# Kernel optimization log

Hardware: AMD Instinct MI355X
Metric: run time of the kernel (lower is better)

The kernel has to match this reference:

```python
import jax, jax.numpy as jnp
import numpy as np
from jax import lax

# Ring of the 8 non-center positions of a 3x3 kernel, cyclic clockwise
# starting at top-middle. A rotation offset 'off' (in 1/8 turns) shifts
# kernel taps around this ring; 'off' = step*rot where step = 8/kernel_rot.
_RING = [(0, 1), (0, 2), (1, 2), (2, 2), (2, 1), (2, 0), (1, 0), (0, 0)]
_CENTER = (1, 1)


def _tap_positions(kernel_type, off):
    """Return list of (row, col) 3x3 positions, one per stored kernel value."""
    if kernel_type == 0:  # skel: 5 taps = 4-point cross (rotated) + center
        pos = [_RING[(2 * k + off) % 8] for k in range(4)] + [_CENTER]
    elif kernel_type == 1:  # full 3x3: 8 ring taps (rotated) + center
        pos = [_RING[(k + off) % 8] for k in range(8)] + [_CENTER]
    else:  # bar: tap - center - opposite tap, rotated
        pos = [_RING[off % 8], _CENTER, _RING[(4 + off) % 8]]
    return pos


def _build_dense_kernel(weight, kernel_type, off):
    # weight: [O, I, num_kernel] -> dense [O, I, 3, 3]
    O, I, nk = weight.shape
    dense = jnp.zeros((O, I, 3, 3), dtype=weight.dtype)
    for k, (r, c) in enumerate(_tap_positions(kernel_type, off)):
        dense = dense.at[:, :, r, c].set(weight[:, :, k])
    return dense


def setup_inputs() -> dict:
    key = jax.random.key(0)
    k1, k2 = jax.random.split(key)
    x_tensor = jax.random.normal(k1, (16, 64, 192, 192), dtype=jnp.float32)
    weight = jax.random.normal(k2, (64, 64, 5), dtype=jnp.float32) * 0.05
    return {"x_tensor": x_tensor, "weight": weight, "rot": 1}


def reference(x_tensor, weight, rot):
    kernel_type = 0          # skel
    kernel_rot = 8
    step = 8 // kernel_rot   # = 1
    off = (step * int(rot)) % 8
    dense = _build_dense_kernel(weight, kernel_type, off)  # [O, I, 3, 3]
    # 3x3 conv, stride 1, padding 1, dilation 1, NCHW/OIHW
    out = lax.conv_general_dilated(
        x_tensor, dense,
        window_strides=(1, 1),
        padding=[(1, 1), (1, 1)],
        rhs_dilation=(1, 1),
        dimension_numbers=("NCHW", "OIHW", "NCHW"),
    )
    return out
```

## Files before the change

kernel.cpp:

```cpp
#include <hip/hip_runtime.h>

#define WD   192
#define HD   192
#define HWD  (WD*HD)
#define NCH  64
#define NOUT 64
#define NK   5
#define BAND 12
#define COLS 194
#define ROWB 128

typedef __attribute__((ext_vector_type(8))) short short8;
typedef __attribute__((ext_vector_type(4))) float f32x4;

__device__ inline ushort f2bf(float f) {
  union { float f; unsigned u; } xx; xx.f = f;
  unsigned u = xx.u;
  return (ushort)((u + 0x7FFFu + ((u >> 16) & 1u)) >> 16);
}

__device__ inline int ldso(int slot, int pix, int cbyte) {
  int byte = (slot * COLS + pix) * ROWB + cbyte;
  return byte ^ ((pix & 7) << 4);
}

__global__ void prep_taps_k(const int* __restrict__ rot, int* __restrict__ taps) {
  const int ring_r[8] = {0,0,1,2,2,2,1,0};
  const int ring_c[8] = {1,2,2,2,1,0,0,0};
  int off = ((rot[0] % 8) + 8) % 8;
  for (int k = 0; k < 4; ++k) {
    int p = (2*k + off) & 7;
    taps[k] = 0; taps[5 + k] = ring_r[p] - 1; taps[10 + k] = ring_c[p] - 1;
  }
  taps[4] = 0; taps[9] = 0; taps[14] = 0;
}

__device__ inline void lds_barrier() {
  __builtin_amdgcn_sched_barrier(0);
  asm volatile("s_waitcnt lgkmcnt(0)" ::: "memory");
  __builtin_amdgcn_sched_barrier(0);
  __builtin_amdgcn_s_barrier();
  __builtin_amdgcn_sched_barrier(0);
}

__global__ __launch_bounds__(512, 2) void rconv_ring_k(
    const float* __restrict__ x, const float* __restrict__ w,
    const int* __restrict__ taps, float* __restrict__ out) {
  __shared__ ushort lds[4 * COLS * (ROWB / 2)];
  char* ldsb = (char*)lds;

  const int tid  = threadIdx.x;
  const int lane = tid & 63;
  const int wv   = tid >> 6;
  const int l15  = lane & 15;
  const int g    = lane >> 4;
  const int r0   = blockIdx.x * BAND;
  const int n    = blockIdx.y;
  const int o0w  = (wv & 1) * 32;
  const int wq   = wv >> 1;

  int dr[NK], dc[NK];
  #pragma unroll
  for (int k = 0; k < NK; ++k) { dr[k] = taps[5 + k]; dc[k] = taps[10 + k]; }

  short8 a[2][2][NK];
  #pragma unroll
  for (int ot = 0; ot < 2; ++ot)
    #pragma unroll
    for (int kc = 0; kc < 2; ++kc)
      #pragma unroll
      for (int k = 0; k < NK; ++k) {
        short8 t;
        #pragma unroll
        for (int j = 0; j < 8; ++j)
          t[j] = (short)f2bf(w[(size_t)(o0w + ot*16 + l15) * (NCH*NK)
                               + (kc*32 + g*8 + j) * NK + k]);
        a[ot][kc][k] = t;
      }

  const float* xn = x + ((size_t)n * NCH + wv * 8) * HWD;

  auto stage_load = [&](int gr, float v[3][8]) {
    bool vr = (gr >= 0) && (gr < HD);
    if (vr) {
      const float* xr = xn + (size_t)gr * WD;
      #pragma unroll
      for (int i = 0; i < 3; ++i)
        #pragma unroll
        for (int j = 0; j < 8; ++j)
          v[i][j] = xr[(size_t)j * HWD + i * 64 + lane];
    } else {
      #pragma unroll
      for (int i = 0; i < 3; ++i)
        #pragma unroll
        for (int j = 0; j < 8; ++j) v[i][j] = 0.f;
    }
  };
  auto stage_write = [&](int gr, const float v[3][8]) {
    int s = gr & 3;
    #pragma unroll
    for (int i = 0; i < 3; ++i) {
      short8 t;
      #pragma unroll
      for (int j = 0; j < 8; ++j) t[j] = (short)f2bf(v[i][j]);
      *reinterpret_cast<short8*>(ldsb + ldso(s, 1 + i * 64 + lane, wv * 16)) = t;
    }
  };

  f32x4 acc[3][2];
  auto compute_row = [&](int r) {
    int bo0[NK], bo1[NK];
    #pragma unroll
    for (int k = 0; k < NK; ++k) {
      int pix = wq * 48 + dc[k] + 1 + l15;
      bo0[k] = ldso((r + dr[k]) & 3, pix, g * 16);
      bo1[k] = ldso((r + dr[k]) & 3, pix, g * 16 + 64);
    }
    #pragma unroll
    for (int t = 0; t < 3; ++t) {
      acc[t][0] = (f32x4){0.f, 0.f, 0.f, 0.f};
      acc[t][1] = (f32x4){0.f, 0.f, 0.f, 0.f};
    }
    __builtin_amdgcn_s_setprio(1);
    #pragma unroll
    for (int t = 0; t < 3; ++t)
      #pragma unroll
      for (int k = 0; k < NK; ++k) {
        short8 b0 = *reinterpret_cast<const short8*>(ldsb + bo0[k] + t * 16 * ROWB);
        short8 b1 = *reinterpret_cast<const short8*>(ldsb + bo1[k] + t * 16 * ROWB);
        acc[t][0] = __builtin_amdgcn_mfma_f32_16x16x32_bf16(b0, a[0][0][k], acc[t][0], 0, 0, 0);
        acc[t][1] = __builtin_amdgcn_mfma_f32_16x16x32_bf16(b0, a[1][0][k], acc[t][1], 0, 0, 0);
        acc[t][0] = __builtin_amdgcn_mfma_f32_16x16x32_bf16(b1, a[0][1][k], acc[t][0], 0, 0, 0);
        acc[t][1] = __builtin_amdgcn_mfma_f32_16x16x32_bf16(b1, a[1][1][k], acc[t][1], 0, 0, 0);
      }
    __builtin_amdgcn_s_setprio(0);
  };
  auto store_row = [&](int r) {
    #pragma unroll
    for (int t = 0; t < 3; ++t)
      #pragma unroll
      for (int ot = 0; ot < 2; ++ot) {
        size_t ob = ((size_t)(n * NOUT + o0w + ot * 16 + l15)) * HWD
                  + (size_t)r * WD + wq * 48 + t * 16 + 4 * g;
        *reinterpret_cast<f32x4*>(&out[ob]) = acc[t][ot];
      }
  };

  float vA[3][8], vB[3][8];

  if (tid < 64) {
    short8 z = (short8){0,0,0,0,0,0,0,0};
    int slot = tid >> 4, px = ((tid >> 3) & 1) * (COLS - 1), cb = (tid & 7) * 16;
    *reinterpret_cast<short8*>(ldsb + ldso(slot, px, cb)) = z;
  }
  stage_load(r0 - 1, vA); stage_write(r0 - 1, vA);
  stage_load(r0,     vA); stage_write(r0,     vA);
  stage_load(r0 + 1, vA); stage_write(r0 + 1, vA);
  stage_load(r0 + 2, vA);
  lds_barrier();

  #pragma unroll 1
  for (int i = 0; i < BAND / 2; ++i) {
    int r = r0 + 2 * i;
    {
      if (r + 3 <= r0 + BAND) stage_load(r + 3, vB);
      compute_row(r);
      stage_write(r + 2, vA);
      lds_barrier();
      store_row(r);
    }
    {
      int r1 = r + 1;
      if (r1 + 3 <= r0 + BAND) stage_load(r1 + 3, vA);
      compute_row(r1);
      if (r1 + 2 <= r0 + BAND) stage_write(r1 + 2, vB);
      lds_barrier();
      store_row(r1);
    }
  }
}

extern "C" void kernel_launch(void* const* d_in, const int* in_sizes, int n_in,
                              void* d_out, int out_size, void* d_ws, size_t ws_size,
                              hipStream_t stream) {
  const float* x = (const float*)d_in[0];
  const float* w = (const float*)d_in[1];
  const int* rot = (const int*)d_in[2];
  float* out     = (float*)d_out;
  int* taps      = (int*)d_ws;

  const int nbatch = in_sizes[0] / (NCH * HWD);

  hipLaunchKernelGGL(prep_taps_k, dim3(1), dim3(1), 0, stream, rot, taps);
  hipLaunchKernelGGL(rconv_ring_k, dim3(HD / BAND, nbatch), dim3(512), 0, stream,
                     x, w, taps, out);
}
```

Before: 78.92 us.

## Repack input to channel-last bf16 and run direct-load MFMA conv without LDS

Adds a pre-pass that converts the fp32 NCHW input into a bf16 NHWC buffer in workspace. A new 1024-thread conv kernel then reads tap rows straight from global memory as 16-byte vectors and feeds MFMA, with no LDS staging or barriers. This removes the LDS ring pipeline and its in-kernel conversion, at the cost of an extra full pass writing and re-reading a bf16 copy of the input (~75MB). Each tap re-reads overlapping rows from global or L2. The old path is kept as a fallback when the workspace is too small.

```diff
diff --git a/kernel.cpp b/kernel.cpp
--- a/kernel.cpp
+++ b/kernel.cpp
@@ -9,6 +9,7 @@
 #define BAND 12
 #define COLS 194
 #define ROWB 128
+#define XBF_OFF 256
 
 typedef __attribute__((ext_vector_type(8))) short short8;
 typedef __attribute__((ext_vector_type(4))) float f32x4;
@@ -43,12 +44,101 @@
   __builtin_amdgcn_sched_barrier(0);
 }
 
+__global__ __launch_bounds__(256) void repack_k(const float* __restrict__ x,
+                                                ushort* __restrict__ xbf) {
+  const int px = blockIdx.x * 256 + threadIdx.x;
+  const int n  = blockIdx.y;
+  const float* xp = x + (size_t)n * NCH * HWD + px;
+  ushort* op = xbf + ((size_t)n * HWD + px) * NCH;
+  #pragma unroll
+  for (int c0 = 0; c0 < NCH; c0 += 16) {
+    short8 b0, b1;
+    #pragma unroll
+    for (int j = 0; j < 8; ++j) b0[j] = (short)f2bf(xp[(size_t)(c0 + j) * HWD]);
+    #pragma unroll
+    for (int j = 0; j < 8; ++j) b1[j] = (short)f2bf(xp[(size_t)(c0 + 8 + j) * HWD]);
+    *reinterpret_cast<short8*>(op + c0)     = b0;
+    *reinterpret_cast<short8*>(op + c0 + 8) = b1;
+  }
+}
+
+__global__ __launch_bounds__(1024, 2) void rconv_direct_k(
+    const ushort* __restrict__ xbf, const float* __restrict__ w,
+    const int* __restrict__ taps, float* __restrict__ out) {
+  const int tid  = threadIdx.x;
+  const int lane = tid & 63;
+  const int wv   = tid >> 6;
+  const int l15  = lane & 15;
+  const int g    = lane >> 4;
+  const int r0   = blockIdx.x * BAND;
+  const int n    = blockIdx.y;
+  const int o0w  = (wv & 3) * 16;
+  const int wq   = wv >> 2;
+
+  int dr[NK], dc[NK];
+  #pragma unroll
+  for (int k = 0; k < NK; ++k) { dr[k] = taps[5 + k]; dc[k] = taps[10 + k]; }
+
+  short8 a[2][NK];
+  #pragma unroll
+  for (int kc = 0; kc < 2; ++kc)
+    #pragma unroll
+    for (int k = 0; k < NK; ++k) {
+      short8 t;
+      #pragma unroll
+      for (int j = 0; j < 8; ++j)
+        t[j] = (short)f2bf(w[(size_t)(o0w + l15) * (NCH*NK)
+                             + (kc*32 + g*8 + j) * NK + k]);
+      a[kc][k] = t;
+    }
+
+  const ushort* xb = xbf + (size_t)n * HWD * NCH;
+
+  #pragma unroll 1
+  for (int r = r0; r < r0 + BAND; ++r) {
+    f32x4 acc[3];
+    #pragma unroll
+    for (int t = 0; t < 3; ++t) acc[t] = (f32x4){0.f, 0.f, 0.f, 0.f};
+
+    #pragma unroll
+    for (int k = 0; k < NK; ++k) {
+      int row = r + dr[k];
+      if ((unsigned)row < (unsigned)HD) {
+        const ushort* rb = xb + (size_t)row * WD * NCH;
+        #pragma unroll
+        for (int t = 0; t < 3; ++t) {
+          int p = wq * 48 + dc[k] + t * 16 + l15;
+          const bool maskable = (wq == 0 && t == 0 && dc[k] < 0) ||
+                                (wq == 3 && t == 2 && dc[k] > 0);
+          int pc = p < 0 ? 0 : (p >= WD ? WD - 1 : p);
+          const ushort* fp = rb + (size_t)pc * NCH + g * 8;
+          short8 b0 = *reinterpret_cast<const short8*>(fp);
+          short8 b1 = *reinterpret_cast<const short8*>(fp + 32);
+          if (maskable) {
+            if (p < 0 || p >= WD) {
+              b0 = (short8){0,0,0,0,0,0,0,0};
+              b1 = (short8){0,0,0,0,0,0,0,0};
+            }
+          }
+          acc[t] = __builtin_amdgcn_mfma_f32_16x16x32_bf16(b0, a[0][k], acc[t], 0, 0, 0);
+          acc[t] = __builtin_amdgcn_mfma_f32_16x16x32_bf16(b1, a[1][k], acc[t], 0, 0, 0);
+        }
+      }
+    }
+    #pragma unroll
+    for (int t = 0; t < 3; ++t) {
+      size_t ob = ((size_t)(n * NOUT + o0w + l15)) * HWD
+                + (size_t)r * WD + wq * 48 + t * 16 + 4 * g;
+      *reinterpret_cast<f32x4*>(&out[ob]) = acc[t];
+    }
+  }
+}
+
 __global__ __launch_bounds__(512, 2) void rconv_ring_k(
     const float* __restrict__ x, const float* __restrict__ w,
     const int* __restrict__ taps, float* __restrict__ out) {
   __shared__ ushort lds[4 * COLS * (ROWB / 2)];
   char* ldsb = (char*)lds;
-
   const int tid  = threadIdx.x;
   const int lane = tid & 63;
   const int wv   = tid >> 6;
@@ -79,7 +169,6 @@
       }
 
   const float* xn = x + ((size_t)n * NCH + wv * 8) * HWD;
-
   auto stage_load = [&](int gr, float v[3][8]) {
     bool vr = (gr >= 0) && (gr < HD);
     if (vr) {
@@ -106,7 +195,6 @@
       *reinterpret_cast<short8*>(ldsb + ldso(s, 1 + i * 64 + lane, wv * 16)) = t;
     }
   };
-
   f32x4 acc[3][2];
   auto compute_row = [&](int r) {
     int bo0[NK], bo1[NK];
@@ -145,9 +233,7 @@
         *reinterpret_cast<f32x4*>(&out[ob]) = acc[t][ot];
       }
   };
-
   float vA[3][8], vB[3][8];
-
   if (tid < 64) {
     short8 z = (short8){0,0,0,0,0,0,0,0};
     int slot = tid >> 4, px = ((tid >> 3) & 1) * (COLS - 1), cb = (tid & 7) * 16;
@@ -158,7 +244,6 @@
   stage_load(r0 + 1, vA); stage_write(r0 + 1, vA);
   stage_load(r0 + 2, vA);
   lds_barrier();
-
   #pragma unroll 1
   for (int i = 0; i < BAND / 2; ++i) {
     int r = r0 + 2 * i;
@@ -190,8 +275,17 @@
   int* taps      = (int*)d_ws;
 
   const int nbatch = in_sizes[0] / (NCH * HWD);
+  const size_t need = (size_t)XBF_OFF + (size_t)nbatch * HWD * NCH * 2;
 
   hipLaunchKernelGGL(prep_taps_k, dim3(1), dim3(1), 0, stream, rot, taps);
-  hipLaunchKernelGGL(rconv_ring_k, dim3(HD / BAND, nbatch), dim3(512), 0, stream,
-                     x, w, taps, out);
-}
+  if (ws_size >= need) {
+    ushort* xbf = (ushort*)((char*)d_ws + XBF_OFF);
+    hipLaunchKernelGGL(repack_k, dim3(HWD / 256, nbatch), dim3(256), 0, stream,
+                       x, xbf);
+    hipLaunchKernelGGL(rconv_direct_k, dim3(HD / BAND, nbatch), dim3(1024), 0,
+                       stream, xbf, w, taps, out);
+  } else {
+    hipLaunchKernelGGL(rconv_ring_k, dim3(HD / BAND, nbatch), dim3(512), 0,
+                       stream, x, w, taps, out);
+  }
+}
```

Result: slower. 253.1 us (+220.7%).
